# Kernel tuning notes

Measured on AMD Instinct MI355X. Metric: run time of the kernel, lower is better.

The kernel has to match this reference:

```python
import jax, jax.numpy as jnp
import numpy as np

NUM_NODES = 64
NUM_FRAMES = 4096
IN_CH = 9
H1 = 256
H2 = 512
NUM_CLASSES = 512
E = 256


def setup_inputs() -> dict:
    key = jax.random.key(0)
    ks = jax.random.split(key, 9)
    x = jax.random.normal(ks[0], (NUM_NODES, NUM_FRAMES, IN_CH), dtype=jnp.float32)
    edge_index = jax.random.randint(ks[1], (2, E), 0, NUM_NODES, dtype=jnp.int64)
    # GCNConv weights (glorot-ish scale) and biases
    W1 = jax.random.normal(ks[2], (IN_CH, H1), dtype=jnp.float32) * (1.0 / np.sqrt(IN_CH))
    b1 = jnp.zeros((H1,), dtype=jnp.float32)
    W2 = jax.random.normal(ks[3], (H1, H2), dtype=jnp.float32) * (1.0 / np.sqrt(H1))
    b2 = jnp.zeros((H2,), dtype=jnp.float32)
    Wfc = jax.random.normal(ks[4], (H2, NUM_CLASSES), dtype=jnp.float32) * (1.0 / np.sqrt(H2))
    bfc = jnp.zeros((NUM_CLASSES,), dtype=jnp.float32)
    return {"x": x, "edge_index": edge_index, "W1": W1, "b1": b1,
            "W2": W2, "b2": b2, "Wfc": Wfc, "bfc": bfc}


def _gcn_layer(x, W, b, src, dst, n):
    # PyG GCNConv: h = X @ W; out_i = sum_j norm_ij * h_j (sym-normalized A + self loops) + b
    h = x @ W  # [N, F_out]
    ones = jnp.ones(src.shape, dtype=h.dtype)
    deg = jax.ops.segment_sum(ones, dst, num_segments=n) + 1.0  # +1 for self-loop
    dis = jax.lax.rsqrt(deg)  # [N]
    norm = dis[src] * dis[dst]  # [E_total]
    agg = jax.ops.segment_sum(h[src] * norm[:, None], dst, num_segments=n)
    agg = agg + h * (dis * dis)[:, None]  # self-loop contribution
    return agg + b


def reference(x, edge_index, W1, b1, W2, b2, Wfc, bfc):
    n_nodes, n_frames, _ = x.shape
    n_total = n_nodes * n_frames
    xf = x.reshape(n_total, -1)
    e = edge_index.shape[1]
    # Tile per-frame edges with per-frame node offsets (block-diagonal graph)
    offs = jnp.repeat(jnp.arange(n_frames, dtype=edge_index.dtype) * n_nodes, e)
    ei = jnp.tile(edge_index, (1, n_frames)) + offs[None, :]
    src, dst = ei[0], ei[1]
    h = jax.nn.relu(_gcn_layer(xf, W1, b1, src, dst, n_total))
    h = jax.nn.relu(_gcn_layer(h, W2, b2, src, dst, n_total))
    feat = h.reshape(n_nodes, n_frames, -1).mean(axis=(0, 1))  # [512]
    return feat @ Wfc + bfc  # [num_classes]
```

## Files before the change

### kernel.cpp

```cpp
#include <hip/hip_runtime.h>

#define NODES   64
#define FRAMES  4096
#define INCH    9
#define H1DIM   256
#define H2DIM   512
#define NEDGE   256
#define CHUNK   64
#define ELLW    16
#define TAILMAX 64

typedef _Float16 half8_t __attribute__((ext_vector_type(8)));
typedef _Float16 half4_t __attribute__((ext_vector_type(4)));
typedef float    f32x16  __attribute__((ext_vector_type(16)));

__global__ void prep_kernel(const int* __restrict__ ei,
                            float* __restrict__ acc,
                            float2* __restrict__ ellG,
                            int* __restrict__ tailCntG,
                            int* __restrict__ tailRowG,
                            int* __restrict__ tailColG,
                            float* __restrict__ tailValG,
                            float* __restrict__ AdenseG)
{
    __shared__ float sA[NODES * NODES];
    __shared__ float dis[NODES];
    __shared__ int   deg[NODES];
    __shared__ int   sTail;
    __shared__ int   flag;
    const int t = threadIdx.x;
    if (t == 0) { flag = 0; sTail = 0; }
    for (int i = t; i < NODES * NODES; i += 256) sA[i] = 0.f;
    if (t < NODES) deg[t] = 1;
    __syncthreads();
    if (ei[2 * t + 1] != 0) atomicOr(&flag, 1);
    __syncthreads();
    const bool is64 = (flag == 0);
    int s = 0, d = 0;
    if (t < NEDGE) {
        if (is64) { s = ei[2 * t];   d = ei[512 + 2 * t]; }
        else      { s = ei[t];       d = ei[NEDGE + t];   }
        atomicAdd(&deg[d], 1);
    }
    __syncthreads();
    if (t < NODES) dis[t] = rsqrtf((float)deg[t]);
    __syncthreads();
    if (t < NEDGE) atomicAdd(&sA[d * NODES + s], dis[s] * dis[d]);
    __syncthreads();
    if (t < NODES) sA[t * NODES + t] += dis[t] * dis[t];
    __syncthreads();
    for (int i = t; i < NODES * NODES; i += 256) AdenseG[i] = sA[i];
    if (t < NODES) {
        int j = 0;
        for (int m = 0; m < NODES; ++m) {
            float v = sA[t * NODES + m];
            if (v != 0.f) {
                if (j < ELLW) {
                    ellG[t * ELLW + j] = make_float2(v, __int_as_float(m));
                } else {
                    int idx = atomicAdd(&sTail, 1);
                    if (idx < TAILMAX) {
                        tailRowG[idx] = t; tailColG[idx] = m; tailValG[idx] = v;
                    }
                }
                ++j;
            }
        }
        for (; j < ELLW; ++j)
            ellG[t * ELLW + j] = make_float2(0.f, __int_as_float(0));
    }
    __syncthreads();
    if (t == 0) *tailCntG = (sTail < TAILMAX) ? sTail : TAILMAX;
    for (int i = t; i < H2DIM; i += 256) acc[i] = 0.f;
}

__global__ void w2frag_kernel(const float* __restrict__ W2,
                              _Float16* __restrict__ w2f)
{
    const int frag = blockIdx.x;
    const int kt = frag >> 4, nt = frag & 15;
    const int l = threadIdx.x;
    const int j = nt * 32 + (l & 31);
    const int kbase = kt * 16 + (l >> 5) * 8;
    const size_t off = (size_t)frag * 1024 + (size_t)l * 16;
    #pragma unroll
    for (int jj = 0; jj < 8; ++jj) {
        float v = W2[(size_t)(kbase + jj) * H2DIM + j];
        _Float16 hv = (_Float16)v;
        w2f[off + jj]     = hv;
        w2f[off + 8 + jj] = (_Float16)(v - (float)hv);
    }
}

__global__ void w1afrag_kernel(const float* __restrict__ W1,
                               const float* __restrict__ Adense,
                               _Float16* __restrict__ w1f,
                               _Float16* __restrict__ af)
{
    const int b = blockIdx.x;
    const int l = threadIdx.x;
    if (b < 8) {
        const size_t off = (size_t)(b * 64 + l) * 16;
        #pragma unroll
        for (int jj = 0; jj < 8; ++jj) {
            const int r = (l >> 5) * 8 + jj;
            float v = (r < INCH) ? W1[r * H1DIM + b * 32 + (l & 31)] : 0.f;
            _Float16 hv = (_Float16)v;
            w1f[off + jj]     = hv;
            w1f[off + 8 + jj] = (_Float16)(v - (float)hv);
        }
    } else {
        const int fa = b - 8;
        const int nt2 = fa >> 2, kt2 = fa & 3;
        const size_t off = (size_t)(fa * 64 + l) * 16;
        #pragma unroll
        for (int jj = 0; jj < 8; ++jj) {
            float v = Adense[(32 * nt2 + (l & 31)) * NODES + 16 * kt2 + (l >> 5) * 8 + jj];
            _Float16 hv = (_Float16)v;
            af[off + jj]     = hv;
            af[off + 8 + jj] = (_Float16)(v - (float)hv);
        }
    }
}

__global__ __launch_bounds__(1024, 4)
void frame_kernel(const float* __restrict__ x,
                  const float2* __restrict__ ellG,
                  const int* __restrict__ tailCntG,
                  const int* __restrict__ tailRowG,
                  const int* __restrict__ tailColG,
                  const float* __restrict__ tailValG,
                  const float* __restrict__ b1,
                  const _Float16* __restrict__ w1f,
                  const _Float16* __restrict__ af,
                  const _Float16* __restrict__ w2f,
                  const float* __restrict__ b2,
                  float* __restrict__ acc)
{
    __shared__ __align__(16) _Float16 sH1f[4][8192];
    __shared__ __align__(16) _Float16 sAH1f[4][4096];
    __shared__ __align__(16) _Float16 sATfH[4096];
    __shared__ __align__(16) _Float16 sATfL[4096];
    __shared__ __align__(16) _Float16 sAXf[2048];
    __shared__ float sPart[H2DIM];
    __shared__ int   sTR[TAILMAX];
    __shared__ int   sTC[TAILMAX];
    __shared__ float sTV[TAILMAX];
    __shared__ int   sTCnt;

    float2 (*sEll)[ELLW] = reinterpret_cast<float2 (*)[ELLW]>(&sH1f[0][0]);
    float (*sX)[12]  = reinterpret_cast<float (*)[12]>(&sH1f[0][4096]);
    float (*sAX)[12] = reinterpret_cast<float (*)[12]>(&sH1f[1][0]);

    const int t   = threadIdx.x;
    const int f   = blockIdx.x;
    const int wv  = t >> 6;
    const int ln  = t & 63;
    const int lh  = ln >> 5, l31 = ln & 31;

    for (int i = t; i < NODES * ELLW; i += 1024)
        sEll[i >> 4][i & 15] = ellG[i];
    if (t == 0) sTCnt = *tailCntG;
    if (t < TAILMAX) { sTR[t] = tailRowG[t]; sTC[t] = tailColG[t]; sTV[t] = tailValG[t]; }
    if (t < H2DIM) sPart[t] = 0.f;
    if (t < 512) {
        const _Float16* ap = af + (size_t)t * 16;
        *(half8_t*)&sATfH[t * 8] = *(const half8_t*)ap;
        *(half8_t*)&sATfL[t * 8] = *(const half8_t*)(ap + 8);
    }
    if (t < NODES * INCH) {
        int n = t / INCH, c = t - n * INCH;
        sX[n][c] = x[(n * FRAMES + f) * INCH + c];
    }
    __syncthreads();

    if (t < NODES * INCH) {
        int n = t / INCH, c = t - n * INCH;
        float v = 0.f;
        #pragma unroll
        for (int jx = 0; jx < ELLW; ++jx) {
            float2 e = sEll[n][jx];
            v = fmaf(e.x, sX[__float_as_int(e.y)][c], v);
        }
        sAX[n][c] = v;
    }
    if (sTCnt > 0) {
        __syncthreads();
        if (t < sTCnt * INCH) {
            int e = t / INCH, c = t - e * INCH;
            atomicAdd(&sAX[sTR[e]][c], sTV[e] * sX[sTC[e]][c]);
        }
    }
    __syncthreads();

    {
        const int row = t >> 4, col = t & 15;
        const float v = (col < INCH) ? sAX[row][col] : 0.f;
        const _Float16 hv = (_Float16)v;
        const _Float16 lv = (_Float16)(v - (float)hv);
        const int idx = (row >> 5) * 512 +
                        (((col >> 3) << 5) | (row & 31)) * 8 + (col & 7);
        sAXf[idx]        = hv;
        sAXf[1024 + idx] = lv;
    }
    __syncthreads();

    {
        const int cc  = wv >> 2;
        const int mtL = (wv >> 1) & 1, ntL = wv & 1;
        const half8_t axh = *(const half8_t*)&sAXf[mtL * 512 + ln * 8];
        const half8_t axl = *(const half8_t*)&sAXf[1024 + mtL * 512 + ln * 8];
        const _Float16* wp = w1f + (size_t)((cc * 2 + ntL) * 64 + ln) * 16;
        const half8_t wh = *(const half8_t*)wp;
        const half8_t wl = *(const half8_t*)(wp + 8);
        f32x16 d;
        #pragma unroll
        for (int q = 0; q < 16; ++q) d[q] = 0.f;
        d = __builtin_amdgcn_mfma_f32_32x32x16_f16(axh, wh, d, 0, 0, 0);
        d = __builtin_amdgcn_mfma_f32_32x32x16_f16(axl, wh, d, 0, 0, 0);
        d = __builtin_amdgcn_mfma_f32_32x32x16_f16(axh, wl, d, 0, 0, 0);
        const float bb = b1[cc * 64 + ntL * 32 + l31];
        _Float16* dst = &sH1f[cc][0];
        #pragma unroll
        for (int j = 0; j < 4; ++j) {
            half4_t hv, lv;
            #pragma unroll
            for (int qq = 0; qq < 4; ++qq) {
                const float v = fmaxf(d[4 * j + qq] + bb, 0.f);
                const _Float16 h = (_Float16)v;
                hv[qq] = h;
                lv[qq] = (_Float16)(v - (float)h);
            }
            const int idx = ((2 * mtL + (j >> 1)) * 2 + ntL) * 512 +
                            (((j & 1) << 5) | l31) * 8 + 4 * lh;
            *(half4_t*)&dst[idx]        = hv;
            *(half4_t*)&dst[4096 + idx] = lv;
        }
    }
    __syncthreads();

    {
        const int cc  = wv >> 2;
        const int mt2 = (wv >> 1) & 1, nt2 = wv & 1;
        const _Float16* src = &sH1f[cc][0];
        f32x16 d0, d1;
        #pragma unroll
        for (int q = 0; q < 16; ++q) { d0[q] = 0.f; d1[q] = 0.f; }
        #pragma unroll
        for (int kt2 = 0; kt2 < 2; ++kt2) {
            const int fb = kt2 * 2 + mt2;
            const half8_t ah = *(const half8_t*)&src[fb * 512 + ln * 8];
            const half8_t al = *(const half8_t*)&src[4096 + fb * 512 + ln * 8];
            const int fa = nt2 * 4 + kt2;
            const half8_t bh = *(const half8_t*)&sATfH[fa * 512 + ln * 8];
            const half8_t bl = *(const half8_t*)&sATfL[fa * 512 + ln * 8];
            d0 = __builtin_amdgcn_mfma_f32_32x32x16_f16(ah, bh, d0, 0, 0, 0);
            d0 = __builtin_amdgcn_mfma_f32_32x32x16_f16(al, bh, d0, 0, 0, 0);
            d0 = __builtin_amdgcn_mfma_f32_32x32x16_f16(ah, bl, d0, 0, 0, 0);
        }
        #pragma unroll
        for (int kt2 = 2; kt2 < 4; ++kt2) {
            const int fb = kt2 * 2 + mt2;
            const half8_t ah = *(const half8_t*)&src[fb * 512 + ln * 8];
            const half8_t al = *(const half8_t*)&src[4096 + fb * 512 + ln * 8];
            const int fa = nt2 * 4 + kt2;
            const half8_t bh = *(const half8_t*)&sATfH[fa * 512 + ln * 8];
            const half8_t bl = *(const half8_t*)&sATfL[fa * 512 + ln * 8];
            d1 = __builtin_amdgcn_mfma_f32_32x32x16_f16(ah, bh, d1, 0, 0, 0);
            d1 = __builtin_amdgcn_mfma_f32_32x32x16_f16(al, bh, d1, 0, 0, 0);
            d1 = __builtin_amdgcn_mfma_f32_32x32x16_f16(ah, bl, d1, 0, 0, 0);
        }
        d0 = d0 + d1;
        _Float16* adst = &sAH1f[cc][0];
        #pragma unroll
        for (int j = 0; j < 4; ++j) {
            half4_t hv;
            #pragma unroll
            for (int qq = 0; qq < 4; ++qq)
                hv[qq] = (_Float16)d0[4 * j + qq];
            const int idx = (nt2 * 4 + 2 * mt2 + (j >> 1)) * 512 +
                            (((j & 1) << 5) | l31) * 8 + 4 * lh;
            *(half4_t*)&adst[idx] = hv;
        }
    }
    __syncthreads();

    f32x16 a2[2];
    #pragma unroll
    for (int q = 0; q < 16; ++q) { a2[0][q] = 0.f; a2[1][q] = 0.f; }
    {
        const _Float16* bp = w2f + (size_t)wv * 1024 + (size_t)ln * 16;
        half8_t bh = *(const half8_t*)bp;
        half8_t bl = *(const half8_t*)(bp + 8);
        #pragma unroll
        for (int ss = 0; ss < 16; ++ss) {
            const int ch = ss >> 2, s = ss & 3;
            half8_t nbh, nbl;
            if (ss < 15) {
                nbh = *(const half8_t*)(bp + 16384);
                nbl = *(const half8_t*)(bp + 16392);
            }
            const _Float16* asrc = &sAH1f[ch][0];
            const half8_t ah0 = *(const half8_t*)&asrc[s * 512 + ln * 8];
            const half8_t ah1 = *(const half8_t*)&asrc[(4 + s) * 512 + ln * 8];
            a2[0] = __builtin_amdgcn_mfma_f32_32x32x16_f16(ah0, bh, a2[0], 0, 0, 0);
            a2[1] = __builtin_amdgcn_mfma_f32_32x32x16_f16(ah1, bh, a2[1], 0, 0, 0);
            a2[0] = __builtin_amdgcn_mfma_f32_32x32x16_f16(ah0, bl, a2[0], 0, 0, 0);
            a2[1] = __builtin_amdgcn_mfma_f32_32x32x16_f16(ah1, bl, a2[1], 0, 0, 0);
            if (ss < 15) { bh = nbh; bl = nbl; bp += 16384; }
        }
    }

    {
        const int j = wv * 32 + l31;
        const float bb = b2[j];
        float ssum = 0.f;
        #pragma unroll
        for (int q = 0; q < 16; ++q) {
            ssum += fmaxf(a2[0][q] + bb, 0.f);
            ssum += fmaxf(a2[1][q] + bb, 0.f);
        }
        atomicAdd(&sPart[j], ssum);
    }
    __syncthreads();
    if (t < H2DIM) atomicAdd(&acc[t], sPart[t]);
}

__global__ void head_kernel(const float* __restrict__ acc,
                            const float* __restrict__ Wfc,
                            const float* __restrict__ bfc,
                            float* __restrict__ out)
{
    const int c = blockIdx.x * 256 + threadIdx.x;
    if (c >= H2DIM) return;
    const float scale = 1.0f / (64.0f * 4096.0f);
    float v = bfc[c];
    for (int j = 0; j < H2DIM; ++j)
        v = fmaf(acc[j] * scale, Wfc[j * H2DIM + c], v);
    out[c] = v;
}

extern "C" void kernel_launch(void* const* d_in, const int* in_sizes, int n_in,
                              void* d_out, int out_size, void* d_ws, size_t ws_size,
                              hipStream_t stream)
{
    const float* x   = (const float*)d_in[0];
    const int*   ei  = (const int*)  d_in[1];
    const float* W1  = (const float*)d_in[2];
    const float* b1  = (const float*)d_in[3];
    const float* W2  = (const float*)d_in[4];
    const float* b2  = (const float*)d_in[5];
    const float* Wfc = (const float*)d_in[6];
    const float* bfc = (const float*)d_in[7];
    float* out = (float*)d_out;

    _Float16* w2f    = (_Float16*)d_ws;
    _Float16* w1f    = w2f + 256 * 1024;
    _Float16* afr    = w1f + 8192;
    float*    Adense = (float*)(afr + 8192);
    float*    acc    = Adense + NODES * NODES;
    float2*   ell    = (float2*)(acc + H2DIM);
    int*   tailCnt   = (int*)(ell + NODES * ELLW);
    int*   tailRow   = tailCnt + 1;
    int*   tailCol   = tailRow + TAILMAX;
    float* tailVal   = (float*)(tailCol + TAILMAX);

    prep_kernel   <<<1,      256,  0, stream>>>(ei, acc, ell, tailCnt,
                                                tailRow, tailCol, tailVal, Adense);
    w2frag_kernel <<<256,     64,  0, stream>>>(W2, w2f);
    w1afrag_kernel<<<16,      64,  0, stream>>>(W1, Adense, w1f, afr);
    frame_kernel  <<<FRAMES, 1024, 0, stream>>>(x, ell, tailCnt,
                                                tailRow, tailCol, tailVal,
                                                b1, w1f, afr, w2f, b2, acc);
    head_kernel   <<<2,      256,  0, stream>>>(acc, Wfc, bfc, out);
}
```

Before: 246.6 us.

## Process sixteen frames per block with a register prefetch of the next frame

Each block now loops over 16 consecutive frames instead of handling one, so the grid shrinks to 256 blocks. Per-block setup is paid once per 16 frames: loading the ELL adjacency, tail edges, A fragments, and the W1 fragments and biases that are now held in registers. Per-frame partial sums stay in registers and are flushed to the global accumulator once per block, cutting global atomics. The next frame's x values are prefetched into registers and written to LDS after a barrier, and the tail-edge correction is folded into the gather, which drops a barrier. The cost is a serial per-block loop that relies on latency hiding within one block per CU, and each wave only reaches the block-wide sum at the end.

```diff
diff --git a/kernel.cpp b/kernel.cpp
--- a/kernel.cpp
+++ b/kernel.cpp
@@ -9,6 +9,7 @@
 #define CHUNK   64
 #define ELLW    16
 #define TAILMAX 64
+#define FPB     16
 
 typedef _Float16 half8_t __attribute__((ext_vector_type(8)));
 typedef _Float16 half4_t __attribute__((ext_vector_type(4)));
@@ -142,18 +143,16 @@
     __shared__ __align__(16) _Float16 sATfH[4096];
     __shared__ __align__(16) _Float16 sATfL[4096];
     __shared__ __align__(16) _Float16 sAXf[2048];
+    __shared__ __align__(16) float2 sEll[NODES][ELLW];
+    __shared__ float sX[NODES][12];
     __shared__ float sPart[H2DIM];
     __shared__ int   sTR[TAILMAX];
     __shared__ int   sTC[TAILMAX];
     __shared__ float sTV[TAILMAX];
     __shared__ int   sTCnt;
 
-    float2 (*sEll)[ELLW] = reinterpret_cast<float2 (*)[ELLW]>(&sH1f[0][0]);
-    float (*sX)[12]  = reinterpret_cast<float (*)[12]>(&sH1f[0][4096]);
-    float (*sAX)[12] = reinterpret_cast<float (*)[12]>(&sH1f[1][0]);
-
     const int t   = threadIdx.x;
-    const int f   = blockIdx.x;
+    const int f0  = blockIdx.x * FPB;
     const int wv  = t >> 6;
     const int ln  = t & 63;
     const int lh  = ln >> 5, l31 = ln & 31;
@@ -170,158 +169,159 @@
     }
     if (t < NODES * INCH) {
         int n = t / INCH, c = t - n * INCH;
-        sX[n][c] = x[(n * FRAMES + f) * INCH + c];
-    }
-    __syncthreads();
-
-    if (t < NODES * INCH) {
-        int n = t / INCH, c = t - n * INCH;
-        float v = 0.f;
-        #pragma unroll
-        for (int jx = 0; jx < ELLW; ++jx) {
-            float2 e = sEll[n][jx];
-            v = fmaf(e.x, sX[__float_as_int(e.y)][c], v);
-        }
-        sAX[n][c] = v;
-    }
-    if (sTCnt > 0) {
+        sX[n][c] = x[((size_t)n * FRAMES + f0) * INCH + c];
+    }
+
+    const int ccP = wv >> 2;
+    const int mtL = (wv >> 1) & 1, ntL = wv & 1;
+    const _Float16* wp = w1f + (size_t)((ccP * 2 + ntL) * 64 + ln) * 16;
+    const half8_t w1h = *(const half8_t*)wp;
+    const half8_t w1l = *(const half8_t*)(wp + 8);
+    const float bb1 = b1[ccP * 64 + ntL * 32 + l31];
+    const float bb2 = b2[wv * 32 + l31];
+    const int rowA = t >> 4, colA = t & 15;
+    const int idxA = (rowA >> 5) * 512 +
+                     (((colA >> 3) << 5) | (rowA & 31)) * 8 + (colA & 7);
+
+    float ssum = 0.f;
+    __syncthreads();
+
+    #pragma unroll 1
+    for (int fr = 0; fr < FPB; ++fr) {
+        float xreg = 0.f;
+        int pn = 0, pc = 0;
+        const bool pf = (t < NODES * INCH) && (fr + 1 < FPB);
+        if (pf) {
+            pn = t / INCH; pc = t - pn * INCH;
+            xreg = x[((size_t)pn * FRAMES + f0 + fr + 1) * INCH + pc];
+        }
+        {
+            float v = 0.f;
+            if (colA < INCH) {
+                #pragma unroll
+                for (int jx = 0; jx < ELLW; ++jx) {
+                    float2 e = sEll[rowA][jx];
+                    v = fmaf(e.x, sX[__float_as_int(e.y)][colA], v);
+                }
+                if (sTCnt > 0) {
+                    #pragma unroll 1
+                    for (int e = 0; e < sTCnt; ++e)
+                        if (sTR[e] == rowA) v += sTV[e] * sX[sTC[e]][colA];
+                }
+            }
+            const _Float16 hv = (_Float16)v;
+            sAXf[idxA]        = hv;
+            sAXf[1024 + idxA] = (_Float16)(v - (float)hv);
+        }
         __syncthreads();
-        if (t < sTCnt * INCH) {
-            int e = t / INCH, c = t - e * INCH;
-            atomicAdd(&sAX[sTR[e]][c], sTV[e] * sX[sTC[e]][c]);
-        }
-    }
-    __syncthreads();
-
-    {
-        const int row = t >> 4, col = t & 15;
-        const float v = (col < INCH) ? sAX[row][col] : 0.f;
-        const _Float16 hv = (_Float16)v;
-        const _Float16 lv = (_Float16)(v - (float)hv);
-        const int idx = (row >> 5) * 512 +
-                        (((col >> 3) << 5) | (row & 31)) * 8 + (col & 7);
-        sAXf[idx]        = hv;
-        sAXf[1024 + idx] = lv;
-    }
-    __syncthreads();
-
-    {
-        const int cc  = wv >> 2;
-        const int mtL = (wv >> 1) & 1, ntL = wv & 1;
-        const half8_t axh = *(const half8_t*)&sAXf[mtL * 512 + ln * 8];
-        const half8_t axl = *(const half8_t*)&sAXf[1024 + mtL * 512 + ln * 8];
-        const _Float16* wp = w1f + (size_t)((cc * 2 + ntL) * 64 + ln) * 16;
-        const half8_t wh = *(const half8_t*)wp;
-        const half8_t wl = *(const half8_t*)(wp + 8);
-        f32x16 d;
-        #pragma unroll
-        for (int q = 0; q < 16; ++q) d[q] = 0.f;
-        d = __builtin_amdgcn_mfma_f32_32x32x16_f16(axh, wh, d, 0, 0, 0);
-        d = __builtin_amdgcn_mfma_f32_32x32x16_f16(axl, wh, d, 0, 0, 0);
-        d = __builtin_amdgcn_mfma_f32_32x32x16_f16(axh, wl, d, 0, 0, 0);
-        const float bb = b1[cc * 64 + ntL * 32 + l31];
-        _Float16* dst = &sH1f[cc][0];
-        #pragma unroll
-        for (int j = 0; j < 4; ++j) {
-            half4_t hv, lv;
-            #pragma unroll
-            for (int qq = 0; qq < 4; ++qq) {
-                const float v = fmaxf(d[4 * j + qq] + bb, 0.f);
-                const _Float16 h = (_Float16)v;
-                hv[qq] = h;
-                lv[qq] = (_Float16)(v - (float)h);
-            }
-            const int idx = ((2 * mtL + (j >> 1)) * 2 + ntL) * 512 +
-                            (((j & 1) << 5) | l31) * 8 + 4 * lh;
-            *(half4_t*)&dst[idx]        = hv;
-            *(half4_t*)&dst[4096 + idx] = lv;
-        }
-    }
-    __syncthreads();
-
-    {
-        const int cc  = wv >> 2;
-        const int mt2 = (wv >> 1) & 1, nt2 = wv & 1;
-        const _Float16* src = &sH1f[cc][0];
-        f32x16 d0, d1;
-        #pragma unroll
-        for (int q = 0; q < 16; ++q) { d0[q] = 0.f; d1[q] = 0.f; }
-        #pragma unroll
-        for (int kt2 = 0; kt2 < 2; ++kt2) {
-            const int fb = kt2 * 2 + mt2;
-            const half8_t ah = *(const half8_t*)&src[fb * 512 + ln * 8];
-            const half8_t al = *(const half8_t*)&src[4096 + fb * 512 + ln * 8];
-            const int fa = nt2 * 4 + kt2;
-            const half8_t bh = *(const half8_t*)&sATfH[fa * 512 + ln * 8];
-            const half8_t bl = *(const half8_t*)&sATfL[fa * 512 + ln * 8];
-            d0 = __builtin_amdgcn_mfma_f32_32x32x16_f16(ah, bh, d0, 0, 0, 0);
-            d0 = __builtin_amdgcn_mfma_f32_32x32x16_f16(al, bh, d0, 0, 0, 0);
-            d0 = __builtin_amdgcn_mfma_f32_32x32x16_f16(ah, bl, d0, 0, 0, 0);
-        }
-        #pragma unroll
-        for (int kt2 = 2; kt2 < 4; ++kt2) {
-            const int fb = kt2 * 2 + mt2;
-            const half8_t ah = *(const half8_t*)&src[fb * 512 + ln * 8];
-            const half8_t al = *(const half8_t*)&src[4096 + fb * 512 + ln * 8];
-            const int fa = nt2 * 4 + kt2;
-            const half8_t bh = *(const half8_t*)&sATfH[fa * 512 + ln * 8];
-            const half8_t bl = *(const half8_t*)&sATfL[fa * 512 + ln * 8];
-            d1 = __builtin_amdgcn_mfma_f32_32x32x16_f16(ah, bh, d1, 0, 0, 0);
-            d1 = __builtin_amdgcn_mfma_f32_32x32x16_f16(al, bh, d1, 0, 0, 0);
-            d1 = __builtin_amdgcn_mfma_f32_32x32x16_f16(ah, bl, d1, 0, 0, 0);
-        }
-        d0 = d0 + d1;
-        _Float16* adst = &sAH1f[cc][0];
-        #pragma unroll
-        for (int j = 0; j < 4; ++j) {
-            half4_t hv;
-            #pragma unroll
-            for (int qq = 0; qq < 4; ++qq)
-                hv[qq] = (_Float16)d0[4 * j + qq];
-            const int idx = (nt2 * 4 + 2 * mt2 + (j >> 1)) * 512 +
-                            (((j & 1) << 5) | l31) * 8 + 4 * lh;
-            *(half4_t*)&adst[idx] = hv;
-        }
-    }
-    __syncthreads();
-
-    f32x16 a2[2];
-    #pragma unroll
-    for (int q = 0; q < 16; ++q) { a2[0][q] = 0.f; a2[1][q] = 0.f; }
-    {
-        const _Float16* bp = w2f + (size_t)wv * 1024 + (size_t)ln * 16;
-        half8_t bh = *(const half8_t*)bp;
-        half8_t bl = *(const half8_t*)(bp + 8);
-        #pragma unroll
-        for (int ss = 0; ss < 16; ++ss) {
-            const int ch = ss >> 2, s = ss & 3;
-            half8_t nbh, nbl;
-            if (ss < 15) {
-                nbh = *(const half8_t*)(bp + 16384);
-                nbl = *(const half8_t*)(bp + 16392);
-            }
-            const _Float16* asrc = &sAH1f[ch][0];
-            const half8_t ah0 = *(const half8_t*)&asrc[s * 512 + ln * 8];
-            const half8_t ah1 = *(const half8_t*)&asrc[(4 + s) * 512 + ln * 8];
-            a2[0] = __builtin_amdgcn_mfma_f32_32x32x16_f16(ah0, bh, a2[0], 0, 0, 0);
-            a2[1] = __builtin_amdgcn_mfma_f32_32x32x16_f16(ah1, bh, a2[1], 0, 0, 0);
-            a2[0] = __builtin_amdgcn_mfma_f32_32x32x16_f16(ah0, bl, a2[0], 0, 0, 0);
-            a2[1] = __builtin_amdgcn_mfma_f32_32x32x16_f16(ah1, bl, a2[1], 0, 0, 0);
-            if (ss < 15) { bh = nbh; bl = nbl; bp += 16384; }
-        }
-    }
-
-    {
-        const int j = wv * 32 + l31;
-        const float bb = b2[j];
-        float ssum = 0.f;
-        #pragma unroll
-        for (int q = 0; q < 16; ++q) {
-            ssum += fmaxf(a2[0][q] + bb, 0.f);
-            ssum += fmaxf(a2[1][q] + bb, 0.f);
-        }
-        atomicAdd(&sPart[j], ssum);
-    }
+
+        if (pf) sX[pn][pc] = xreg;
+        {
+            const half8_t axh = *(const half8_t*)&sAXf[mtL * 512 + ln * 8];
+            const half8_t axl = *(const half8_t*)&sAXf[1024 + mtL * 512 + ln * 8];
+            f32x16 d;
+            #pragma unroll
+            for (int q = 0; q < 16; ++q) d[q] = 0.f;
+            d = __builtin_amdgcn_mfma_f32_32x32x16_f16(axh, w1h, d, 0, 0, 0);
+            d = __builtin_amdgcn_mfma_f32_32x32x16_f16(axl, w1h, d, 0, 0, 0);
+            d = __builtin_amdgcn_mfma_f32_32x32x16_f16(axh, w1l, d, 0, 0, 0);
+            _Float16* dst = &sH1f[ccP][0];
+            #pragma unroll
+            for (int j = 0; j < 4; ++j) {
+                half4_t hv, lv;
+                #pragma unroll
+                for (int qq = 0; qq < 4; ++qq) {
+                    const float v = fmaxf(d[4 * j + qq] + bb1, 0.f);
+                    const _Float16 h = (_Float16)v;
+                    hv[qq] = h;
+                    lv[qq] = (_Float16)(v - (float)h);
+                }
+                const int idx = ((2 * mtL + (j >> 1)) * 2 + ntL) * 512 +
+                                (((j & 1) << 5) | l31) * 8 + 4 * lh;
+                *(half4_t*)&dst[idx]        = hv;
+                *(half4_t*)&dst[4096 + idx] = lv;
+            }
+        }
+        __syncthreads();
+
+        {
+            const _Float16* src = &sH1f[ccP][0];
+            f32x16 d0, d1;
+            #pragma unroll
+            for (int q = 0; q < 16; ++q) { d0[q] = 0.f; d1[q] = 0.f; }
+            #pragma unroll
+            for (int kt2 = 0; kt2 < 2; ++kt2) {
+                const int fb = kt2 * 2 + mtL;
+                const half8_t ah = *(const half8_t*)&src[fb * 512 + ln * 8];
+                const half8_t al = *(const half8_t*)&src[4096 + fb * 512 + ln * 8];
+                const int fa = ntL * 4 + kt2;
+                const half8_t bh = *(const half8_t*)&sATfH[fa * 512 + ln * 8];
+                const half8_t bl = *(const half8_t*)&sATfL[fa * 512 + ln * 8];
+                d0 = __builtin_amdgcn_mfma_f32_32x32x16_f16(ah, bh, d0, 0, 0, 0);
+                d0 = __builtin_amdgcn_mfma_f32_32x32x16_f16(al, bh, d0, 0, 0, 0);
+                d0 = __builtin_amdgcn_mfma_f32_32x32x16_f16(ah, bl, d0, 0, 0, 0);
+            }
+            #pragma unroll
+            for (int kt2 = 2; kt2 < 4; ++kt2) {
+                const int fb = kt2 * 2 + mtL;
+                const half8_t ah = *(const half8_t*)&src[fb * 512 + ln * 8];
+                const half8_t al = *(const half8_t*)&src[4096 + fb * 512 + ln * 8];
+                const int fa = ntL * 4 + kt2;
+                const half8_t bh = *(const half8_t*)&sATfH[fa * 512 + ln * 8];
+                const half8_t bl = *(const half8_t*)&sATfL[fa * 512 + ln * 8];
+                d1 = __builtin_amdgcn_mfma_f32_32x32x16_f16(ah, bh, d1, 0, 0, 0);
+                d1 = __builtin_amdgcn_mfma_f32_32x32x16_f16(al, bh, d1, 0, 0, 0);
+                d1 = __builtin_amdgcn_mfma_f32_32x32x16_f16(ah, bl, d1, 0, 0, 0);
+            }
+            d0 = d0 + d1;
+            _Float16* adst = &sAH1f[ccP][0];
+            #pragma unroll
+            for (int j = 0; j < 4; ++j) {
+                half4_t hv;
+                #pragma unroll
+                for (int qq = 0; qq < 4; ++qq)
+                    hv[qq] = (_Float16)d0[4 * j + qq];
+                const int idx = (ntL * 4 + 2 * mtL + (j >> 1)) * 512 +
+                                (((j & 1) << 5) | l31) * 8 + 4 * lh;
+                *(half4_t*)&adst[idx] = hv;
+            }
+        }
+        __syncthreads();
+
+        {
+            f32x16 a2[2];
+            #pragma unroll
+            for (int q = 0; q < 16; ++q) { a2[0][q] = 0.f; a2[1][q] = 0.f; }
+            const _Float16* bp = w2f + (size_t)wv * 1024 + (size_t)ln * 16;
+            half8_t bh = *(const half8_t*)bp;
+            half8_t bl = *(const half8_t*)(bp + 8);
+            #pragma unroll
+            for (int ss = 0; ss < 16; ++ss) {
+                const int ch = ss >> 2, s = ss & 3;
+                half8_t nbh, nbl;
+                if (ss < 15) {
+                    nbh = *(const half8_t*)(bp + 16384);
+                    nbl = *(const half8_t*)(bp + 16392);
+                }
+                const _Float16* asrc = &sAH1f[ch][0];
+                const half8_t ah0 = *(const half8_t*)&asrc[s * 512 + ln * 8];
+                const half8_t ah1 = *(const half8_t*)&asrc[(4 + s) * 512 + ln * 8];
+                a2[0] = __builtin_amdgcn_mfma_f32_32x32x16_f16(ah0, bh, a2[0], 0, 0, 0);
+                a2[1] = __builtin_amdgcn_mfma_f32_32x32x16_f16(ah1, bh, a2[1], 0, 0, 0);
+                a2[0] = __builtin_amdgcn_mfma_f32_32x32x16_f16(ah0, bl, a2[0], 0, 0, 0);
+                a2[1] = __builtin_amdgcn_mfma_f32_32x32x16_f16(ah1, bl, a2[1], 0, 0, 0);
+                if (ss < 15) { bh = nbh; bl = nbl; bp += 16384; }
+            }
+            #pragma unroll
+            for (int q = 0; q < 16; ++q) {
+                ssum += fmaxf(a2[0][q] + bb2, 0.f);
+                ssum += fmaxf(a2[1][q] + bb2, 0.f);
+            }
+        }
+        __syncthreads();
+    }
+
+    atomicAdd(&sPart[wv * 32 + l31], ssum);
     __syncthreads();
     if (t < H2DIM) atomicAdd(&acc[t], sPart[t]);
 }
@@ -369,8 +369,8 @@
                                                 tailRow, tailCol, tailVal, Adense);
     w2frag_kernel <<<256,     64,  0, stream>>>(W2, w2f);
     w1afrag_kernel<<<16,      64,  0, stream>>>(W1, Adense, w1f, afr);
-    frame_kernel  <<<FRAMES, 1024, 0, stream>>>(x, ell, tailCnt,
-                                                tailRow, tailCol, tailVal,
-                                                b1, w1f, afr, w2f, b2, acc);
+    frame_kernel  <<<FRAMES / FPB, 1024, 0, stream>>>(x, ell, tailCnt,
+                                                      tailRow, tailCol, tailVal,
+                                                      b1, w1f, afr, w2f, b2, acc);
     head_kernel   <<<2,      256,  0, stream>>>(acc, Wfc, bfc, out);
 }
```

New measurement: 303.1 us. 1.23x slower.

## Process two frames per block to reuse W2 fragments and drop H1 low-part split

Applied to the files above, without the earlier changes.

Each block now handles two frames, so every W2 fragment loaded from global memory feeds MFMAs for both frames, halving W2 traffic per frame and doubling MFMA work per load. The layer-1 output is stored only as a single fp16 value instead of a hi/lo split, which removes one MFMA per step in the A·H1 product and halves that LDS storage. The cost is lower accuracy for H1, larger LDS use (sAH1f doubled), more accumulator registers and half as many blocks.

```diff
diff --git a/kernel.cpp b/kernel.cpp
--- a/kernel.cpp
+++ b/kernel.cpp
@@ -137,23 +137,22 @@
                   const float* __restrict__ b2,
                   float* __restrict__ acc)
 {
-    __shared__ __align__(16) _Float16 sH1f[4][8192];
-    __shared__ __align__(16) _Float16 sAH1f[4][4096];
+    __shared__ __align__(16) float2 sEll[NODES][ELLW];
+    __shared__ float sX [2][NODES][12];
+    __shared__ float sAX[2][NODES][12];
+    __shared__ __align__(16) _Float16 sAXf[2][2048];
+    __shared__ __align__(16) _Float16 sH1f[4][4096];
+    __shared__ __align__(16) _Float16 sAH1f[2][4][4096];
     __shared__ __align__(16) _Float16 sATfH[4096];
     __shared__ __align__(16) _Float16 sATfL[4096];
-    __shared__ __align__(16) _Float16 sAXf[2048];
     __shared__ float sPart[H2DIM];
     __shared__ int   sTR[TAILMAX];
     __shared__ int   sTC[TAILMAX];
     __shared__ float sTV[TAILMAX];
     __shared__ int   sTCnt;
 
-    float2 (*sEll)[ELLW] = reinterpret_cast<float2 (*)[ELLW]>(&sH1f[0][0]);
-    float (*sX)[12]  = reinterpret_cast<float (*)[12]>(&sH1f[0][4096]);
-    float (*sAX)[12] = reinterpret_cast<float (*)[12]>(&sH1f[1][0]);
-
     const int t   = threadIdx.x;
-    const int f   = blockIdx.x;
+    const int f0  = blockIdx.x * 2;
     const int wv  = t >> 6;
     const int ln  = t & 63;
     const int lh  = ln >> 5, l31 = ln & 31;
@@ -168,48 +167,56 @@
         *(half8_t*)&sATfH[t * 8] = *(const half8_t*)ap;
         *(half8_t*)&sATfL[t * 8] = *(const half8_t*)(ap + 8);
     }
-    if (t < NODES * INCH) {
-        int n = t / INCH, c = t - n * INCH;
-        sX[n][c] = x[(n * FRAMES + f) * INCH + c];
-    }
-    __syncthreads();
-
-    if (t < NODES * INCH) {
-        int n = t / INCH, c = t - n * INCH;
+    for (int i = t; i < 2 * NODES * INCH; i += 1024) {
+        const int ff = i / (NODES * INCH);
+        const int r  = i - ff * (NODES * INCH);
+        const int n  = r / INCH, c = r - n * INCH;
+        sX[ff][n][c] = x[((size_t)n * FRAMES + f0 + ff) * INCH + c];
+    }
+    __syncthreads();
+
+    for (int i = t; i < 2 * NODES * INCH; i += 1024) {
+        const int ff = i / (NODES * INCH);
+        const int r  = i - ff * (NODES * INCH);
+        const int n  = r / INCH, c = r - n * INCH;
         float v = 0.f;
         #pragma unroll
         for (int jx = 0; jx < ELLW; ++jx) {
             float2 e = sEll[n][jx];
-            v = fmaf(e.x, sX[__float_as_int(e.y)][c], v);
-        }
-        sAX[n][c] = v;
+            v = fmaf(e.x, sX[ff][__float_as_int(e.y)][c], v);
+        }
+        sAX[ff][n][c] = v;
     }
     if (sTCnt > 0) {
         __syncthreads();
-        if (t < sTCnt * INCH) {
-            int e = t / INCH, c = t - e * INCH;
-            atomicAdd(&sAX[sTR[e]][c], sTV[e] * sX[sTC[e]][c]);
-        }
-    }
-    __syncthreads();
-
-    {
-        const int row = t >> 4, col = t & 15;
-        const float v = (col < INCH) ? sAX[row][col] : 0.f;
+        for (int i = t; i < 2 * sTCnt * INCH; i += 1024) {
+            const int ff = i / (sTCnt * INCH);
+            const int r  = i - ff * (sTCnt * INCH);
+            const int e  = r / INCH, c = r - e * INCH;
+            atomicAdd(&sAX[ff][sTR[e]][c], sTV[e] * sX[ff][sTC[e]][c]);
+        }
+    }
+    __syncthreads();
+
+    for (int i = t; i < 2048; i += 1024) {
+        const int ff  = i >> 10;
+        const int ii  = i & 1023;
+        const int row = ii >> 4, col = ii & 15;
+        const float v = (col < INCH) ? sAX[ff][row][col] : 0.f;
         const _Float16 hv = (_Float16)v;
         const _Float16 lv = (_Float16)(v - (float)hv);
         const int idx = (row >> 5) * 512 +
                         (((col >> 3) << 5) | (row & 31)) * 8 + (col & 7);
-        sAXf[idx]        = hv;
-        sAXf[1024 + idx] = lv;
-    }
-    __syncthreads();
-
-    {
+        sAXf[ff][idx]        = hv;
+        sAXf[ff][1024 + idx] = lv;
+    }
+    __syncthreads();
+
+    auto P1 = [&](int ff) {
         const int cc  = wv >> 2;
         const int mtL = (wv >> 1) & 1, ntL = wv & 1;
-        const half8_t axh = *(const half8_t*)&sAXf[mtL * 512 + ln * 8];
-        const half8_t axl = *(const half8_t*)&sAXf[1024 + mtL * 512 + ln * 8];
+        const half8_t axh = *(const half8_t*)&sAXf[ff][mtL * 512 + ln * 8];
+        const half8_t axl = *(const half8_t*)&sAXf[ff][1024 + mtL * 512 + ln * 8];
         const _Float16* wp = w1f + (size_t)((cc * 2 + ntL) * 64 + ln) * 16;
         const half8_t wh = *(const half8_t*)wp;
         const half8_t wl = *(const half8_t*)(wp + 8);
@@ -223,23 +230,17 @@
         _Float16* dst = &sH1f[cc][0];
         #pragma unroll
         for (int j = 0; j < 4; ++j) {
-            half4_t hv, lv;
+            half4_t hv;
             #pragma unroll
-            for (int qq = 0; qq < 4; ++qq) {
-                const float v = fmaxf(d[4 * j + qq] + bb, 0.f);
-                const _Float16 h = (_Float16)v;
-                hv[qq] = h;
-                lv[qq] = (_Float16)(v - (float)h);
-            }
+            for (int qq = 0; qq < 4; ++qq)
+                hv[qq] = (_Float16)fmaxf(d[4 * j + qq] + bb, 0.f);
             const int idx = ((2 * mtL + (j >> 1)) * 2 + ntL) * 512 +
                             (((j & 1) << 5) | l31) * 8 + 4 * lh;
-            *(half4_t*)&dst[idx]        = hv;
-            *(half4_t*)&dst[4096 + idx] = lv;
-        }
-    }
-    __syncthreads();
-
-    {
+            *(half4_t*)&dst[idx] = hv;
+        }
+    };
+
+    auto P2 = [&](int ff) {
         const int cc  = wv >> 2;
         const int mt2 = (wv >> 1) & 1, nt2 = wv & 1;
         const _Float16* src = &sH1f[cc][0];
@@ -250,28 +251,24 @@
         for (int kt2 = 0; kt2 < 2; ++kt2) {
             const int fb = kt2 * 2 + mt2;
             const half8_t ah = *(const half8_t*)&src[fb * 512 + ln * 8];
-            const half8_t al = *(const half8_t*)&src[4096 + fb * 512 + ln * 8];
             const int fa = nt2 * 4 + kt2;
             const half8_t bh = *(const half8_t*)&sATfH[fa * 512 + ln * 8];
             const half8_t bl = *(const half8_t*)&sATfL[fa * 512 + ln * 8];
             d0 = __builtin_amdgcn_mfma_f32_32x32x16_f16(ah, bh, d0, 0, 0, 0);
-            d0 = __builtin_amdgcn_mfma_f32_32x32x16_f16(al, bh, d0, 0, 0, 0);
             d0 = __builtin_amdgcn_mfma_f32_32x32x16_f16(ah, bl, d0, 0, 0, 0);
         }
         #pragma unroll
         for (int kt2 = 2; kt2 < 4; ++kt2) {
             const int fb = kt2 * 2 + mt2;
             const half8_t ah = *(const half8_t*)&src[fb * 512 + ln * 8];
-            const half8_t al = *(const half8_t*)&src[4096 + fb * 512 + ln * 8];
             const int fa = nt2 * 4 + kt2;
             const half8_t bh = *(const half8_t*)&sATfH[fa * 512 + ln * 8];
             const half8_t bl = *(const half8_t*)&sATfL[fa * 512 + ln * 8];
             d1 = __builtin_amdgcn_mfma_f32_32x32x16_f16(ah, bh, d1, 0, 0, 0);
-            d1 = __builtin_amdgcn_mfma_f32_32x32x16_f16(al, bh, d1, 0, 0, 0);
             d1 = __builtin_amdgcn_mfma_f32_32x32x16_f16(ah, bl, d1, 0, 0, 0);
         }
         d0 = d0 + d1;
-        _Float16* adst = &sAH1f[cc][0];
+        _Float16* adst = &sAH1f[ff][cc][0];
         #pragma unroll
         for (int j = 0; j < 4; ++j) {
             half4_t hv;
@@ -282,12 +279,23 @@
                             (((j & 1) << 5) | l31) * 8 + 4 * lh;
             *(half4_t*)&adst[idx] = hv;
         }
-    }
-    __syncthreads();
-
-    f32x16 a2[2];
+    };
+
+    P1(0);
+    __syncthreads();
+    P2(0);
+    __syncthreads();
+    P1(1);
+    __syncthreads();
+    P2(1);
+    __syncthreads();
+
+    f32x16 a2[2][2];
     #pragma unroll
-    for (int q = 0; q < 16; ++q) { a2[0][q] = 0.f; a2[1][q] = 0.f; }
+    for (int q = 0; q < 16; ++q) {
+        a2[0][0][q] = 0.f; a2[0][1][q] = 0.f;
+        a2[1][0][q] = 0.f; a2[1][1][q] = 0.f;
+    }
     {
         const _Float16* bp = w2f + (size_t)wv * 1024 + (size_t)ln * 16;
         half8_t bh = *(const half8_t*)bp;
@@ -300,27 +308,35 @@
                 nbh = *(const half8_t*)(bp + 16384);
                 nbl = *(const half8_t*)(bp + 16392);
             }
-            const _Float16* asrc = &sAH1f[ch][0];
-            const half8_t ah0 = *(const half8_t*)&asrc[s * 512 + ln * 8];
-            const half8_t ah1 = *(const half8_t*)&asrc[(4 + s) * 512 + ln * 8];
-            a2[0] = __builtin_amdgcn_mfma_f32_32x32x16_f16(ah0, bh, a2[0], 0, 0, 0);
-            a2[1] = __builtin_amdgcn_mfma_f32_32x32x16_f16(ah1, bh, a2[1], 0, 0, 0);
-            a2[0] = __builtin_amdgcn_mfma_f32_32x32x16_f16(ah0, bl, a2[0], 0, 0, 0);
-            a2[1] = __builtin_amdgcn_mfma_f32_32x32x16_f16(ah1, bl, a2[1], 0, 0, 0);
+            const _Float16* a0 = &sAH1f[0][ch][0];
+            const _Float16* a1 = &sAH1f[1][ch][0];
+            const half8_t f0m0 = *(const half8_t*)&a0[s * 512 + ln * 8];
+            const half8_t f0m1 = *(const half8_t*)&a0[(4 + s) * 512 + ln * 8];
+            const half8_t f1m0 = *(const half8_t*)&a1[s * 512 + ln * 8];
+            const half8_t f1m1 = *(const half8_t*)&a1[(4 + s) * 512 + ln * 8];
+            a2[0][0] = __builtin_amdgcn_mfma_f32_32x32x16_f16(f0m0, bh, a2[0][0], 0, 0, 0);
+            a2[0][1] = __builtin_amdgcn_mfma_f32_32x32x16_f16(f0m1, bh, a2[0][1], 0, 0, 0);
+            a2[1][0] = __builtin_amdgcn_mfma_f32_32x32x16_f16(f1m0, bh, a2[1][0], 0, 0, 0);
+            a2[1][1] = __builtin_amdgcn_mfma_f32_32x32x16_f16(f1m1, bh, a2[1][1], 0, 0, 0);
+            a2[0][0] = __builtin_amdgcn_mfma_f32_32x32x16_f16(f0m0, bl, a2[0][0], 0, 0, 0);
+            a2[0][1] = __builtin_amdgcn_mfma_f32_32x32x16_f16(f0m1, bl, a2[0][1], 0, 0, 0);
+            a2[1][0] = __builtin_amdgcn_mfma_f32_32x32x16_f16(f1m0, bl, a2[1][0], 0, 0, 0);
+            a2[1][1] = __builtin_amdgcn_mfma_f32_32x32x16_f16(f1m1, bl, a2[1][1], 0, 0, 0);
             if (ss < 15) { bh = nbh; bl = nbl; bp += 16384; }
         }
     }
 
     {
-        const int j = wv * 32 + l31;
-        const float bb = b2[j];
+        const float bb = b2[wv * 32 + l31];
         float ssum = 0.f;
         #pragma unroll
         for (int q = 0; q < 16; ++q) {
-            ssum += fmaxf(a2[0][q] + bb, 0.f);
-            ssum += fmaxf(a2[1][q] + bb, 0.f);
-        }
-        atomicAdd(&sPart[j], ssum);
+            ssum += fmaxf(a2[0][0][q] + bb, 0.f);
+            ssum += fmaxf(a2[0][1][q] + bb, 0.f);
+            ssum += fmaxf(a2[1][0][q] + bb, 0.f);
+            ssum += fmaxf(a2[1][1][q] + bb, 0.f);
+        }
+        atomicAdd(&sPart[wv * 32 + l31], ssum);
     }
     __syncthreads();
     if (t < H2DIM) atomicAdd(&acc[t], sPart[t]);
@@ -365,12 +381,12 @@
     int*   tailCol   = tailRow + TAILMAX;
     float* tailVal   = (float*)(tailCol + TAILMAX);
 
-    prep_kernel   <<<1,      256,  0, stream>>>(ei, acc, ell, tailCnt,
-                                                tailRow, tailCol, tailVal, Adense);
-    w2frag_kernel <<<256,     64,  0, stream>>>(W2, w2f);
-    w1afrag_kernel<<<16,      64,  0, stream>>>(W1, Adense, w1f, afr);
-    frame_kernel  <<<FRAMES, 1024, 0, stream>>>(x, ell, tailCnt,
-                                                tailRow, tailCol, tailVal,
-                                                b1, w1f, afr, w2f, b2, acc);
-    head_kernel   <<<2,      256,  0, stream>>>(acc, Wfc, bfc, out);
-}
+    prep_kernel   <<<1,           256,  0, stream>>>(ei, acc, ell, tailCnt,
+                                                     tailRow, tailCol, tailVal, Adense);
+    w2frag_kernel <<<256,          64,  0, stream>>>(W2, w2f);
+    w1afrag_kernel<<<16,           64,  0, stream>>>(W1, Adense, w1f, afr);
+    frame_kernel  <<<FRAMES / 2, 1024,  0, stream>>>(x, ell, tailCnt,
+                                                     tailRow, tailCol, tailVal,
+                                                     b1, w1f, afr, w2f, b2, acc);
+    head_kernel   <<<2,           256,  0, stream>>>(acc, Wfc, bfc, out);
+}
```

Measured after the change: 201.8 us (median of 2 runs). 18.2% less time.
